# Kernel tuning notes

Hardware: AMD Instinct MI355X
Metric: run time of the kernel (lower is better)

## Reference

```python
import jax, jax.numpy as jnp
import numpy as np

N_NODES = 100000


def setup_inputs() -> dict:
    key = jax.random.key(0)
    k1, k2, k3, k4, k5, k6 = jax.random.split(key, 6)
    n_edges = 1600000
    X = jax.random.normal(k1, (N_NODES, 256), dtype=jnp.float32)
    edge_row = jax.random.randint(k2, (n_edges,), 0, N_NODES, dtype=jnp.int64)
    edge_col = jax.random.randint(k3, (n_edges,), 0, N_NODES, dtype=jnp.int64)
    edge_val = jax.random.uniform(k4, (n_edges,), dtype=jnp.float32)
    W = jax.random.normal(k5, (128, 256), dtype=jnp.float32) * 0.05
    b = jax.random.normal(k6, (128,), dtype=jnp.float32) * 0.05
    return {"X": X, "edge_row": edge_row, "edge_col": edge_col,
            "edge_val": edge_val, "W": W, "b": b}


def reference(X, edge_row, edge_col, edge_val, W, b):
    # Dense projection: H = X @ W^T + b  -> [N, out_dim]
    H = jnp.einsum('ni,oi->no', X, W) + b
    # SpMM: out[r] = sum_e A[r, c_e] * H[c_e] over edges with row r
    msgs = edge_val[:, None] * H[edge_col]          # [E, out_dim]
    out = jax.ops.segment_sum(msgs, edge_row, num_segments=N_NODES)
    return out
```

## Files before the change

### kernel.cpp

```cpp
#include <hip/hip_runtime.h>
#include <hip/hip_bf16.h>

#define NNODES 100000
#define NEDGES 1600000
#define KDIM 256
#define ODIM 128
#define NXCD 8
#define NB_SCAN 391
#define EDGE_CAP 1900032
#define GEMM_BLOCKS 1563
#define RANK_BLOCKS 1563
#define CONV_BLOCKS 128

typedef __attribute__((ext_vector_type(8))) short short8;
typedef __attribute__((ext_vector_type(4))) float floatx4;

static __device__ __forceinline__ short f2bf(float f) {
  union { float f; unsigned u; } x; x.f = f;
  unsigned r = (x.u + 0x7fffu + ((x.u >> 16) & 1u)) >> 16;
  return (short)r;
}

__global__ __launch_bounds__(256) void conv_rank_kernel(
    const float* __restrict__ W, short* __restrict__ Wb,
    const int* __restrict__ rows, unsigned* __restrict__ counts,
    unsigned short* __restrict__ rank) {
  if (blockIdx.x < CONV_BLOCKS) {
    int i = blockIdx.x * 256 + threadIdx.x;
    if (i < ODIM * KDIM) Wb[i] = f2bf(W[i]);
    return;
  }
  unsigned xcc;
  asm("s_getreg_b32 %0, hwreg(HW_REG_XCC_ID)" : "=s"(xcc));
  xcc &= 7u;
  unsigned* cbase = counts + (size_t)xcc * NNODES;
  const int e0 = ((blockIdx.x - CONV_BLOCKS) * 256 + threadIdx.x) * 4;
  if (e0 < NEDGES) {
    const int4 r4 = *(const int4*)(rows + e0);
    const unsigned o0 = __hip_atomic_fetch_add(&cbase[r4.x], 1u, __ATOMIC_RELAXED,
                                               __HIP_MEMORY_SCOPE_WORKGROUP);
    const unsigned o1 = __hip_atomic_fetch_add(&cbase[r4.y], 1u, __ATOMIC_RELAXED,
                                               __HIP_MEMORY_SCOPE_WORKGROUP);
    const unsigned o2 = __hip_atomic_fetch_add(&cbase[r4.z], 1u, __ATOMIC_RELAXED,
                                               __HIP_MEMORY_SCOPE_WORKGROUP);
    const unsigned o3 = __hip_atomic_fetch_add(&cbase[r4.w], 1u, __ATOMIC_RELAXED,
                                               __HIP_MEMORY_SCOPE_WORKGROUP);
    ushort4 rk;
    rk.x = (unsigned short)((xcc << 8) | o0);
    rk.y = (unsigned short)((xcc << 8) | o1);
    rk.z = (unsigned short)((xcc << 8) | o2);
    rk.w = (unsigned short)((xcc << 8) | o3);
    *(ushort4*)(rank + e0) = rk;
  }
}

__global__ __launch_bounds__(256) void gemm_scan1_kernel(
    const float* __restrict__ X, const short* __restrict__ Wb,
    const float* __restrict__ bias, unsigned* __restrict__ H2,
    const unsigned* __restrict__ counts, int* __restrict__ chunkExcl,
    int* __restrict__ blockSums) {
  __shared__ int s[256];
  if (blockIdx.x < NB_SCAN) {
    int t = threadIdx.x;
    int n = blockIdx.x * 256 + t;
    int sum = 0;
    if (n < NNODES) {
      int s0 = 0;
#pragma unroll
      for (int x = 0; x < NXCD; x++) s0 += (int)counts[(size_t)x * NNODES + n];
      sum = (s0 + 3) & ~3;
    }
    s[t] = sum;
    __syncthreads();
    for (int o = 1; o < 256; o <<= 1) {
      int add = (t >= o) ? s[t - o] : 0;
      __syncthreads();
      s[t] += add;
      __syncthreads();
    }
    if (n < NNODES) chunkExcl[n] = s[t] - sum;
    if (t == 255) blockSums[blockIdx.x] = s[255];
    return;
  }
  const int gb = blockIdx.x - NB_SCAN;
  const int lane = threadIdx.x & 63;
  const int wave = threadIdx.x >> 6;
  const int l16 = lane & 15;
  const int quad = lane >> 4;
  const int rowBase = gb * 64 + wave * 16;
  const int arow = rowBase + l16;
  const bool inb = arow < NNODES;
  const float4 zf4 = {0.f, 0.f, 0.f, 0.f};
  const float4* xp = (const float4*)(X + (size_t)(inb ? arow : 0) * KDIM + quad * 8);

  floatx4 acc[8];
#pragma unroll
  for (int t = 0; t < 8; t++) acc[t] = (floatx4){0.f, 0.f, 0.f, 0.f};

  float4 c0 = inb ? xp[0] : zf4;
  float4 c1 = inb ? xp[1] : zf4;
#pragma unroll
  for (int k0 = 0; k0 < 8; k0++) {
    float4 n0, n1;
    if (k0 < 7) {
      n0 = inb ? xp[(k0 + 1) * 8] : zf4;
      n1 = inb ? xp[(k0 + 1) * 8 + 1] : zf4;
    }
    short8 a;
    a[0] = f2bf(c0.x); a[1] = f2bf(c0.y); a[2] = f2bf(c0.z); a[3] = f2bf(c0.w);
    a[4] = f2bf(c1.x); a[5] = f2bf(c1.y); a[6] = f2bf(c1.z); a[7] = f2bf(c1.w);
    const short* bp = Wb + k0 * 32 + quad * 8;
#pragma unroll
    for (int t = 0; t < 8; t++) {
      short8 b = *(const short8*)(bp + (size_t)(t * 16 + l16) * KDIM);
      acc[t] = __builtin_amdgcn_mfma_f32_16x16x32_bf16(a, b, acc[t], 0, 0, 0);
    }
    if (k0 < 7) { c0 = n0; c1 = n1; }
  }

#pragma unroll
  for (int t = 0; t < 4; t++) {
    const int cl = t * 16 + l16;
    const float blo = bias[cl];
    const float bhi = bias[cl + 64];
#pragma unroll
    for (int r = 0; r < 4; r++) {
      const int row = rowBase + quad * 4 + r;
      if (row < NNODES) {
        unsigned lo = (unsigned short)f2bf(acc[t][r] + blo);
        unsigned hi = (unsigned short)f2bf(acc[t + 4][r] + bhi);
        H2[(size_t)row * 64 + cl] = lo | (hi << 16);
      }
    }
  }
}

__global__ __launch_bounds__(512) void scan23_kernel(
    const int* __restrict__ blockSums, const int* __restrict__ chunkExcl,
    unsigned* __restrict__ counts, int* __restrict__ offsets,
    int2* __restrict__ edges) {
  __shared__ int s[512];
  const int t = threadIdx.x;
  s[t] = (t < NB_SCAN) ? blockSums[t] : 0;
  __syncthreads();
  for (int o = 1; o < 512; o <<= 1) {
    int add = (t >= o) ? s[t - o] : 0;
    __syncthreads();
    s[t] += add;
    __syncthreads();
  }
  const int myBase = (blockIdx.x == 0) ? 0 : s[blockIdx.x - 1];
  if (blockIdx.x == 0 && t == 0) offsets[NNODES] = s[NB_SCAN - 1];
  if (t < 256) {
    const int n = blockIdx.x * 256 + t;
    if (n < NNODES) {
      const int run = chunkExcl[n] + myBase;
      offsets[n] = run;
      int c[NXCD];
      int deg = 0;
#pragma unroll
      for (int x = 0; x < NXCD; x++) {
        c[x] = (int)counts[(size_t)x * NNODES + n];
        deg += c[x];
      }
      int acc2 = run;
#pragma unroll
      for (int x = 0; x < NXCD; x++) {
        counts[(size_t)x * NNODES + n] = (unsigned)acc2;
        acc2 += c[x];
      }
      const int padded = (deg + 3) & ~3;
      const int2 zrec = {0, 0};
      for (int p = run + deg; p < run + padded; p++) edges[p] = zrec;
    }
  }
}

__global__ __launch_bounds__(256) void place_kernel(
    const int* __restrict__ rows, const int* __restrict__ cols,
    const float* __restrict__ vals, const unsigned short* __restrict__ rank,
    const unsigned* __restrict__ sbase, int2* __restrict__ edges) {
  const int e0 = (blockIdx.x * 256 + threadIdx.x) * 4;
  if (e0 < NEDGES) {
    const int4 r4 = *(const int4*)(rows + e0);
    const int4 c4 = *(const int4*)(cols + e0);
    const float4 v4 = *(const float4*)(vals + e0);
    const ushort4 k4 = *(const ushort4*)(rank + e0);
    int2 rec;
    rec.x = c4.x; rec.y = __float_as_int(v4.x);
    edges[(int)sbase[(size_t)(k4.x >> 8) * NNODES + r4.x] + (int)(k4.x & 255u)] = rec;
    rec.x = c4.y; rec.y = __float_as_int(v4.y);
    edges[(int)sbase[(size_t)(k4.y >> 8) * NNODES + r4.y] + (int)(k4.y & 255u)] = rec;
    rec.x = c4.z; rec.y = __float_as_int(v4.z);
    edges[(int)sbase[(size_t)(k4.z >> 8) * NNODES + r4.z] + (int)(k4.z & 255u)] = rec;
    rec.x = c4.w; rec.y = __float_as_int(v4.w);
    edges[(int)sbase[(size_t)(k4.w >> 8) * NNODES + r4.w] + (int)(k4.w & 255u)] = rec;
  }
}

__global__ __launch_bounds__(256) void spmm_kernel(const int* __restrict__ offsets,
                                                   const int2* __restrict__ edges,
                                                   const unsigned* __restrict__ H2,
                                                   float* __restrict__ out) {
  const int lane = threadIdx.x & 63;
  const int row = blockIdx.x * 4 + (threadIdx.x >> 6);
  if (row >= NNODES) return;
  const int s = offsets[row];
  const int e = offsets[row + 1];
  float ax = 0.f, ay = 0.f;
  for (int i = s; i < e; i += 4) {
    const int4 p01 = *(const int4*)(edges + i);
    const int4 p23 = *(const int4*)(edges + i + 2);
    const unsigned h0 = H2[(size_t)p01.x * 64 + lane];
    const unsigned h1 = H2[(size_t)p01.z * 64 + lane];
    const unsigned h2 = H2[(size_t)p23.x * 64 + lane];
    const unsigned h3 = H2[(size_t)p23.z * 64 + lane];
    const float v0 = __int_as_float(p01.y);
    const float v1 = __int_as_float(p01.w);
    const float v2 = __int_as_float(p23.y);
    const float v3 = __int_as_float(p23.w);
    ax += v0 * __uint_as_float(h0 << 16);
    ay += v0 * __uint_as_float(h0 & 0xffff0000u);
    ax += v1 * __uint_as_float(h1 << 16);
    ay += v1 * __uint_as_float(h1 & 0xffff0000u);
    ax += v2 * __uint_as_float(h2 << 16);
    ay += v2 * __uint_as_float(h2 & 0xffff0000u);
    ax += v3 * __uint_as_float(h3 << 16);
    ay += v3 * __uint_as_float(h3 & 0xffff0000u);
  }
  out[(size_t)row * 128 + lane] = ax;
  out[(size_t)row * 128 + 64 + lane] = ay;
}

extern "C" void kernel_launch(void* const* d_in, const int* in_sizes, int n_in,
                              void* d_out, int out_size, void* d_ws, size_t ws_size,
                              hipStream_t stream) {
  const float* X = (const float*)d_in[0];
  const int* erow = (const int*)d_in[1];
  const int* ecol = (const int*)d_in[2];
  const float* eval = (const float*)d_in[3];
  const float* W = (const float*)d_in[4];
  const float* bias = (const float*)d_in[5];
  float* out = (float*)d_out;

  char* ws = (char*)d_ws;
  size_t off = 0;
  auto alloc = [&](size_t bytes) -> char* {
    char* p = ws + off;
    off += (bytes + 255) & ~(size_t)255;
    return p;
  };
  unsigned* Hb = (unsigned*)alloc((size_t)NNODES * 64 * 4);
  short* Wb = (short*)alloc((size_t)ODIM * KDIM * 2);
  unsigned* counts = (unsigned*)alloc((size_t)NXCD * NNODES * 4);
  int* chunkExcl = (int*)alloc((size_t)NNODES * 4);
  int* offsets = (int*)alloc((size_t)(NNODES + 1) * 4);
  int* blockSums = (int*)alloc((size_t)NB_SCAN * 4);
  unsigned short* rank = (unsigned short*)alloc((size_t)NEDGES * 2);
  int2* edges = (int2*)alloc((size_t)EDGE_CAP * 8);

  hipMemsetAsync(counts, 0, (size_t)NXCD * NNODES * 4, stream);
  conv_rank_kernel<<<CONV_BLOCKS + RANK_BLOCKS, 256, 0, stream>>>(W, Wb, erow, counts, rank);
  gemm_scan1_kernel<<<NB_SCAN + GEMM_BLOCKS, 256, 0, stream>>>(X, Wb, bias, Hb,
                                                               counts, chunkExcl, blockSums);
  scan23_kernel<<<NB_SCAN, 512, 0, stream>>>(blockSums, chunkExcl, counts, offsets, edges);
  place_kernel<<<RANK_BLOCKS, 256, 0, stream>>>(erow, ecol, eval, rank, counts, edges);
  spmm_kernel<<<(NNODES + 3) / 4, 256, 0, stream>>>(offsets, edges, (const unsigned*)Hb, out);
}
```

Measured before the change: 398.7 us.

## Replace rank array with atomic cursor placement and co-schedule GEMM with edge placement

The histogram pass no longer records a per-edge rank. Edge placement now takes its slot by atomically incrementing per-XCC cursors, which are initialised from the scanned counts. That placement work is fused into the same launch as the bf16 MFMA GEMM, so the scatter overlaps the dense projection, while scan1 becomes a standalone kernel. This removes the rank array write and read, at the cost of a second round of atomics and a nondeterministic edge order within each row (floating-point summation order varies). It also relies on each block landing on the same XCC in both launches.

```diff
diff --git a/kernel.cpp b/kernel.cpp
--- a/kernel.cpp
+++ b/kernel.cpp
@@ -9,7 +9,7 @@
 #define NB_SCAN 391
 #define EDGE_CAP 1900032
 #define GEMM_BLOCKS 1563
-#define RANK_BLOCKS 1563
+#define EDGE_BLOCKS 1563
 #define CONV_BLOCKS 128
 
 typedef __attribute__((ext_vector_type(8))) short short8;
@@ -21,10 +21,9 @@
   return (short)r;
 }
 
-__global__ __launch_bounds__(256) void conv_rank_kernel(
+__global__ __launch_bounds__(256) void conv_hist_kernel(
     const float* __restrict__ W, short* __restrict__ Wb,
-    const int* __restrict__ rows, unsigned* __restrict__ counts,
-    unsigned short* __restrict__ rank) {
+    const int* __restrict__ rows, unsigned* __restrict__ counts) {
   if (blockIdx.x < CONV_BLOCKS) {
     int i = blockIdx.x * 256 + threadIdx.x;
     if (i < ODIM * KDIM) Wb[i] = f2bf(W[i]);
@@ -37,102 +36,36 @@
   const int e0 = ((blockIdx.x - CONV_BLOCKS) * 256 + threadIdx.x) * 4;
   if (e0 < NEDGES) {
     const int4 r4 = *(const int4*)(rows + e0);
-    const unsigned o0 = __hip_atomic_fetch_add(&cbase[r4.x], 1u, __ATOMIC_RELAXED,
-                                               __HIP_MEMORY_SCOPE_WORKGROUP);
-    const unsigned o1 = __hip_atomic_fetch_add(&cbase[r4.y], 1u, __ATOMIC_RELAXED,
-                                               __HIP_MEMORY_SCOPE_WORKGROUP);
-    const unsigned o2 = __hip_atomic_fetch_add(&cbase[r4.z], 1u, __ATOMIC_RELAXED,
-                                               __HIP_MEMORY_SCOPE_WORKGROUP);
-    const unsigned o3 = __hip_atomic_fetch_add(&cbase[r4.w], 1u, __ATOMIC_RELAXED,
-                                               __HIP_MEMORY_SCOPE_WORKGROUP);
-    ushort4 rk;
-    rk.x = (unsigned short)((xcc << 8) | o0);
-    rk.y = (unsigned short)((xcc << 8) | o1);
-    rk.z = (unsigned short)((xcc << 8) | o2);
-    rk.w = (unsigned short)((xcc << 8) | o3);
-    *(ushort4*)(rank + e0) = rk;
-  }
-}
-
-__global__ __launch_bounds__(256) void gemm_scan1_kernel(
-    const float* __restrict__ X, const short* __restrict__ Wb,
-    const float* __restrict__ bias, unsigned* __restrict__ H2,
+    __hip_atomic_fetch_add(&cbase[r4.x], 1u, __ATOMIC_RELAXED, __HIP_MEMORY_SCOPE_WORKGROUP);
+    __hip_atomic_fetch_add(&cbase[r4.y], 1u, __ATOMIC_RELAXED, __HIP_MEMORY_SCOPE_WORKGROUP);
+    __hip_atomic_fetch_add(&cbase[r4.z], 1u, __ATOMIC_RELAXED, __HIP_MEMORY_SCOPE_WORKGROUP);
+    __hip_atomic_fetch_add(&cbase[r4.w], 1u, __ATOMIC_RELAXED, __HIP_MEMORY_SCOPE_WORKGROUP);
+  }
+}
+
+__global__ __launch_bounds__(256) void scan1_kernel(
     const unsigned* __restrict__ counts, int* __restrict__ chunkExcl,
     int* __restrict__ blockSums) {
   __shared__ int s[256];
-  if (blockIdx.x < NB_SCAN) {
-    int t = threadIdx.x;
-    int n = blockIdx.x * 256 + t;
-    int sum = 0;
-    if (n < NNODES) {
-      int s0 = 0;
-#pragma unroll
-      for (int x = 0; x < NXCD; x++) s0 += (int)counts[(size_t)x * NNODES + n];
-      sum = (s0 + 3) & ~3;
-    }
-    s[t] = sum;
-    __syncthreads();
-    for (int o = 1; o < 256; o <<= 1) {
-      int add = (t >= o) ? s[t - o] : 0;
-      __syncthreads();
-      s[t] += add;
-      __syncthreads();
-    }
-    if (n < NNODES) chunkExcl[n] = s[t] - sum;
-    if (t == 255) blockSums[blockIdx.x] = s[255];
-    return;
-  }
-  const int gb = blockIdx.x - NB_SCAN;
-  const int lane = threadIdx.x & 63;
-  const int wave = threadIdx.x >> 6;
-  const int l16 = lane & 15;
-  const int quad = lane >> 4;
-  const int rowBase = gb * 64 + wave * 16;
-  const int arow = rowBase + l16;
-  const bool inb = arow < NNODES;
-  const float4 zf4 = {0.f, 0.f, 0.f, 0.f};
-  const float4* xp = (const float4*)(X + (size_t)(inb ? arow : 0) * KDIM + quad * 8);
-
-  floatx4 acc[8];
-#pragma unroll
-  for (int t = 0; t < 8; t++) acc[t] = (floatx4){0.f, 0.f, 0.f, 0.f};
-
-  float4 c0 = inb ? xp[0] : zf4;
-  float4 c1 = inb ? xp[1] : zf4;
-#pragma unroll
-  for (int k0 = 0; k0 < 8; k0++) {
-    float4 n0, n1;
-    if (k0 < 7) {
-      n0 = inb ? xp[(k0 + 1) * 8] : zf4;
-      n1 = inb ? xp[(k0 + 1) * 8 + 1] : zf4;
-    }
-    short8 a;
-    a[0] = f2bf(c0.x); a[1] = f2bf(c0.y); a[2] = f2bf(c0.z); a[3] = f2bf(c0.w);
-    a[4] = f2bf(c1.x); a[5] = f2bf(c1.y); a[6] = f2bf(c1.z); a[7] = f2bf(c1.w);
-    const short* bp = Wb + k0 * 32 + quad * 8;
-#pragma unroll
-    for (int t = 0; t < 8; t++) {
-      short8 b = *(const short8*)(bp + (size_t)(t * 16 + l16) * KDIM);
-      acc[t] = __builtin_amdgcn_mfma_f32_16x16x32_bf16(a, b, acc[t], 0, 0, 0);
-    }
-    if (k0 < 7) { c0 = n0; c1 = n1; }
-  }
-
-#pragma unroll
-  for (int t = 0; t < 4; t++) {
-    const int cl = t * 16 + l16;
-    const float blo = bias[cl];
-    const float bhi = bias[cl + 64];
-#pragma unroll
-    for (int r = 0; r < 4; r++) {
-      const int row = rowBase + quad * 4 + r;
-      if (row < NNODES) {
-        unsigned lo = (unsigned short)f2bf(acc[t][r] + blo);
-        unsigned hi = (unsigned short)f2bf(acc[t + 4][r] + bhi);
-        H2[(size_t)row * 64 + cl] = lo | (hi << 16);
-      }
-    }
-  }
+  int t = threadIdx.x;
+  int n = blockIdx.x * 256 + t;
+  int sum = 0;
+  if (n < NNODES) {
+    int s0 = 0;
+#pragma unroll
+    for (int x = 0; x < NXCD; x++) s0 += (int)counts[(size_t)x * NNODES + n];
+    sum = (s0 + 3) & ~3;
+  }
+  s[t] = sum;
+  __syncthreads();
+  for (int o = 1; o < 256; o <<= 1) {
+    int add = (t >= o) ? s[t - o] : 0;
+    __syncthreads();
+    s[t] += add;
+    __syncthreads();
+  }
+  if (n < NNODES) chunkExcl[n] = s[t] - sum;
+  if (t == 255) blockSums[blockIdx.x] = s[255];
 }
 
 __global__ __launch_bounds__(512) void scan23_kernel(
@@ -176,25 +109,85 @@
   }
 }
 
-__global__ __launch_bounds__(256) void place_kernel(
+__global__ __launch_bounds__(256) void gemm_place_kernel(
+    const float* __restrict__ X, const short* __restrict__ Wb,
+    const float* __restrict__ bias, unsigned* __restrict__ H2,
     const int* __restrict__ rows, const int* __restrict__ cols,
-    const float* __restrict__ vals, const unsigned short* __restrict__ rank,
-    const unsigned* __restrict__ sbase, int2* __restrict__ edges) {
-  const int e0 = (blockIdx.x * 256 + threadIdx.x) * 4;
-  if (e0 < NEDGES) {
-    const int4 r4 = *(const int4*)(rows + e0);
-    const int4 c4 = *(const int4*)(cols + e0);
-    const float4 v4 = *(const float4*)(vals + e0);
-    const ushort4 k4 = *(const ushort4*)(rank + e0);
-    int2 rec;
-    rec.x = c4.x; rec.y = __float_as_int(v4.x);
-    edges[(int)sbase[(size_t)(k4.x >> 8) * NNODES + r4.x] + (int)(k4.x & 255u)] = rec;
-    rec.x = c4.y; rec.y = __float_as_int(v4.y);
-    edges[(int)sbase[(size_t)(k4.y >> 8) * NNODES + r4.y] + (int)(k4.y & 255u)] = rec;
-    rec.x = c4.z; rec.y = __float_as_int(v4.z);
-    edges[(int)sbase[(size_t)(k4.z >> 8) * NNODES + r4.z] + (int)(k4.z & 255u)] = rec;
-    rec.x = c4.w; rec.y = __float_as_int(v4.w);
-    edges[(int)sbase[(size_t)(k4.w >> 8) * NNODES + r4.w] + (int)(k4.w & 255u)] = rec;
+    const float* __restrict__ vals, unsigned* __restrict__ cursor,
+    int2* __restrict__ edges) {
+  if (blockIdx.x < EDGE_BLOCKS) {
+    unsigned xcc;
+    asm("s_getreg_b32 %0, hwreg(HW_REG_XCC_ID)" : "=s"(xcc));
+    xcc &= 7u;
+    unsigned* cur = cursor + (size_t)xcc * NNODES;
+    const int e0 = (blockIdx.x * 256 + threadIdx.x) * 4;
+    if (e0 < NEDGES) {
+      const int4 r4 = *(const int4*)(rows + e0);
+      const int4 c4 = *(const int4*)(cols + e0);
+      const float4 v4 = *(const float4*)(vals + e0);
+      int2 rec;
+      unsigned p;
+      p = __hip_atomic_fetch_add(&cur[r4.x], 1u, __ATOMIC_RELAXED, __HIP_MEMORY_SCOPE_WORKGROUP);
+      rec.x = c4.x; rec.y = __float_as_int(v4.x); edges[p] = rec;
+      p = __hip_atomic_fetch_add(&cur[r4.y], 1u, __ATOMIC_RELAXED, __HIP_MEMORY_SCOPE_WORKGROUP);
+      rec.x = c4.y; rec.y = __float_as_int(v4.y); edges[p] = rec;
+      p = __hip_atomic_fetch_add(&cur[r4.z], 1u, __ATOMIC_RELAXED, __HIP_MEMORY_SCOPE_WORKGROUP);
+      rec.x = c4.z; rec.y = __float_as_int(v4.z); edges[p] = rec;
+      p = __hip_atomic_fetch_add(&cur[r4.w], 1u, __ATOMIC_RELAXED, __HIP_MEMORY_SCOPE_WORKGROUP);
+      rec.x = c4.w; rec.y = __float_as_int(v4.w); edges[p] = rec;
+    }
+    return;
+  }
+  const int gb = blockIdx.x - EDGE_BLOCKS;
+  const int lane = threadIdx.x & 63;
+  const int wave = threadIdx.x >> 6;
+  const int l16 = lane & 15;
+  const int quad = lane >> 4;
+  const int rowBase = gb * 64 + wave * 16;
+  const int arow = rowBase + l16;
+  const bool inb = arow < NNODES;
+  const float4 zf4 = {0.f, 0.f, 0.f, 0.f};
+  const float4* xp = (const float4*)(X + (size_t)(inb ? arow : 0) * KDIM + quad * 8);
+
+  floatx4 acc[8];
+#pragma unroll
+  for (int t = 0; t < 8; t++) acc[t] = (floatx4){0.f, 0.f, 0.f, 0.f};
+
+  float4 c0 = inb ? xp[0] : zf4;
+  float4 c1 = inb ? xp[1] : zf4;
+#pragma unroll
+  for (int k0 = 0; k0 < 8; k0++) {
+    float4 n0, n1;
+    if (k0 < 7) {
+      n0 = inb ? xp[(k0 + 1) * 8] : zf4;
+      n1 = inb ? xp[(k0 + 1) * 8 + 1] : zf4;
+    }
+    short8 a;
+    a[0] = f2bf(c0.x); a[1] = f2bf(c0.y); a[2] = f2bf(c0.z); a[3] = f2bf(c0.w);
+    a[4] = f2bf(c1.x); a[5] = f2bf(c1.y); a[6] = f2bf(c1.z); a[7] = f2bf(c1.w);
+    const short* bp = Wb + k0 * 32 + quad * 8;
+#pragma unroll
+    for (int t = 0; t < 8; t++) {
+      short8 b = *(const short8*)(bp + (size_t)(t * 16 + l16) * KDIM);
+      acc[t] = __builtin_amdgcn_mfma_f32_16x16x32_bf16(a, b, acc[t], 0, 0, 0);
+    }
+    if (k0 < 7) { c0 = n0; c1 = n1; }
+  }
+
+#pragma unroll
+  for (int t = 0; t < 4; t++) {
+    const int cl = t * 16 + l16;
+    const float blo = bias[cl];
+    const float bhi = bias[cl + 64];
+#pragma unroll
+    for (int r = 0; r < 4; r++) {
+      const int row = rowBase + quad * 4 + r;
+      if (row < NNODES) {
+        unsigned lo = (unsigned short)f2bf(acc[t][r] + blo);
+        unsigned hi = (unsigned short)f2bf(acc[t + 4][r] + bhi);
+        H2[(size_t)row * 64 + cl] = lo | (hi << 16);
+      }
+    }
   }
 }
 
@@ -256,14 +249,13 @@
   int* chunkExcl = (int*)alloc((size_t)NNODES * 4);
   int* offsets = (int*)alloc((size_t)(NNODES + 1) * 4);
   int* blockSums = (int*)alloc((size_t)NB_SCAN * 4);
-  unsigned short* rank = (unsigned short*)alloc((size_t)NEDGES * 2);
   int2* edges = (int2*)alloc((size_t)EDGE_CAP * 8);
 
   hipMemsetAsync(counts, 0, (size_t)NXCD * NNODES * 4, stream);
-  conv_rank_kernel<<<CONV_BLOCKS + RANK_BLOCKS, 256, 0, stream>>>(W, Wb, erow, counts, rank);
-  gemm_scan1_kernel<<<NB_SCAN + GEMM_BLOCKS, 256, 0, stream>>>(X, Wb, bias, Hb,
-                                                               counts, chunkExcl, blockSums);
+  conv_hist_kernel<<<CONV_BLOCKS + EDGE_BLOCKS, 256, 0, stream>>>(W, Wb, erow, counts);
+  scan1_kernel<<<NB_SCAN, 256, 0, stream>>>(counts, chunkExcl, blockSums);
   scan23_kernel<<<NB_SCAN, 512, 0, stream>>>(blockSums, chunkExcl, counts, offsets, edges);
-  place_kernel<<<RANK_BLOCKS, 256, 0, stream>>>(erow, ecol, eval, rank, counts, edges);
+  gemm_place_kernel<<<EDGE_BLOCKS + GEMM_BLOCKS, 256, 0, stream>>>(
+      X, Wb, bias, Hb, erow, ecol, eval, counts, edges);
   spmm_kernel<<<(NNODES + 3) / 4, 256, 0, stream>>>(offsets, edges, (const unsigned*)Hb, out);
 }
```

After: 461.0 us. 1.16x slower.
